# Performance work log

Hardware: AMD Instinct MI355X
Metric: run time of the kernel (lower is better)

## Reference

```python
import jax, jax.numpy as jnp
import numpy as np

NX = 96
N_NODES = 6 * NX * NX          # 55296 cubed-sphere grid points
N_EDGES = 4 * N_NODES          # ~4-neighbor connectivity
HID = 32
NUM_STEPS = 3


def setup_inputs() -> dict:
    key = jax.random.key(0)
    ks = jax.random.split(key, 12)
    s = 0.05
    inp = {
        "in_node_features": jax.random.normal(ks[0], (2, 6, NX, NX, 32), jnp.float32),
        "edge_relation": jax.random.normal(ks[1], (N_EDGES, 4), jnp.float32),
        "pw1": jax.random.normal(ks[2], (32, HID), jnp.float32) * s,
        "pb1": jnp.zeros((HID,), jnp.float32),
        "pw2": jax.random.normal(ks[3], (HID, HID), jnp.float32) * s,
        "pb2": jnp.zeros((HID,), jnp.float32),
        "ew1": jax.random.normal(ks[4], (4, 32), jnp.float32) * s,
        "eb1": jnp.zeros((32,), jnp.float32),
        "ew2": jax.random.normal(ks[5], (32, HID * HID), jnp.float32) * s,
        "eb2": jnp.zeros((HID * HID,), jnp.float32),
        "conv_b": jnp.zeros((HID,), jnp.float32),
        "gru_w_ih": jax.random.normal(ks[6], (3 * HID, HID), jnp.float32) * s,
        "gru_w_hh": jax.random.normal(ks[7], (3 * HID, HID), jnp.float32) * s,
        "gru_b_ih": jnp.zeros((3 * HID,), jnp.float32),
        "gru_b_hh": jnp.zeros((3 * HID,), jnp.float32),
        "edge_src": jax.random.randint(ks[8], (N_EDGES,), 0, N_NODES, jnp.int32),
        "edge_dst": jax.random.randint(ks[9], (N_EDGES,), 0, N_NODES, jnp.int32),
    }
    return inp


def reference(in_node_features, edge_relation, pw1, pb1, pw2, pb2,
              ew1, eb1, ew2, eb2, conv_b,
              gru_w_ih, gru_w_hh, gru_b_ih, gru_b_hh,
              edge_src, edge_dst):
    B, T, nx1, nx2, C = in_node_features.shape
    N = T * nx1 * nx2
    H = pw2.shape[1]

    x = in_node_features.reshape(B, N, C)
    # project_node_features: Linear -> ReLU -> Linear
    h0 = jnp.maximum(x @ pw1 + pb1, 0.0) @ pw2 + pb2          # [B, N, H]

    # edge network (same every step): Linear -> ReLU -> Linear -> [E, H, H]
    We = (jnp.maximum(edge_relation @ ew1 + eb1, 0.0) @ ew2 + eb2)
    We = We.reshape(-1, H, H)                                  # [E, H, H]

    def seg_sum(m):  # m: [E, H] -> [N, H]
        return jax.ops.segment_sum(m, edge_dst, num_segments=N)

    def step(carry, _):
        node, hidden = carry                                   # each [B, N, H]
        # NNConv: gather src feats, per-edge matmul, scatter-sum to dst
        msg = jnp.einsum('beh,eho->beo', node[:, edge_src], We)  # [B, E, H]
        agg = jax.vmap(seg_sum)(msg) + conv_b                    # [B, N, H]
        node = jnp.maximum(agg, 0.0)                             # ReLU
        # single GRU step (seq_len = 1)
        gx = node @ gru_w_ih.T + gru_b_ih                        # [B, N, 3H]
        gh = hidden @ gru_w_hh.T + gru_b_hh
        r = jax.nn.sigmoid(gx[..., :H] + gh[..., :H])
        z = jax.nn.sigmoid(gx[..., H:2 * H] + gh[..., H:2 * H])
        n = jnp.tanh(gx[..., 2 * H:] + r * gh[..., 2 * H:])
        hidden = (1.0 - z) * n + z * hidden
        return (hidden, hidden), None

    (node, _), _ = jax.lax.scan(step, (h0, h0), None, length=NUM_STEPS)
    return node.reshape(B, T, nx1, nx2, H)
```

## Files before the change

### kernel.cpp

```cpp
#include <hip/hip_runtime.h>

typedef unsigned short u16;
typedef short s16x8 __attribute__((ext_vector_type(8)));
typedef float f32x4 __attribute__((ext_vector_type(4)));
typedef float f32x2 __attribute__((ext_vector_type(2)));

#define NNODES 55296
#define NEDGES 221184
#define ROWS   110592
#define NBLK_SCAN 216

__device__ __forceinline__ u16 f2bf(float f) {
    union { float f; unsigned u; } v; v.f = f;
    unsigned r = (v.u + 0x7fffu + ((v.u >> 16) & 1u)) >> 16;
    return (u16)r;
}
__device__ __forceinline__ float bf2f(u16 u) {
    return __uint_as_float(((unsigned)u) << 16);
}

__global__ __launch_bounds__(256) void hist_kernel(
    const int* __restrict__ edst, int* __restrict__ cnt)
{
    int i = blockIdx.x * 256 + threadIdx.x;
    atomicAdd(&cnt[edst[i]], 1);
}

__global__ __launch_bounds__(256) void scan1_kernel(
    const int* __restrict__ cnt, int* __restrict__ exc, int* __restrict__ bsum)
{
    __shared__ int s[256];
    int t = threadIdx.x, g = blockIdx.x * 256 + t;
    int v = cnt[g];
    s[t] = v; __syncthreads();
#pragma unroll
    for (int d = 1; d < 256; d <<= 1) {
        int x = (t >= d) ? s[t - d] : 0;
        __syncthreads();
        s[t] += x;
        __syncthreads();
    }
    exc[g] = s[t] - v;
    if (t == 255) bsum[blockIdx.x] = s[255];
}

__global__ __launch_bounds__(256) void scan2_kernel(
    const int* __restrict__ bsum, int* __restrict__ bofs)
{
    __shared__ int s[256];
    int t = threadIdx.x;
    int v = (t < NBLK_SCAN) ? bsum[t] : 0;
    s[t] = v; __syncthreads();
#pragma unroll
    for (int d = 1; d < 256; d <<= 1) {
        int x = (t >= d) ? s[t - d] : 0;
        __syncthreads();
        s[t] += x;
        __syncthreads();
    }
    if (t < NBLK_SCAN) bofs[t] = s[t] - v;
}

__global__ __launch_bounds__(256) void scan3_kernel(
    const int* __restrict__ exc, const int* __restrict__ bofs, int* __restrict__ rowstart)
{
    int g = blockIdx.x * 256 + threadIdx.x;
    rowstart[g] = exc[g] + bofs[blockIdx.x];
    if (g == 0) rowstart[NNODES] = NEDGES;
}

__global__ __launch_bounds__(256) void scatter_kernel(
    const int* __restrict__ edst, const int* __restrict__ esrc,
    const int* __restrict__ rowstart, int* __restrict__ cursor,
    int* __restrict__ perm, int* __restrict__ esrcp, int* __restrict__ edstp)
{
    int i = blockIdx.x * 256 + threadIdx.x;
    int d = edst[i];
    int pos = rowstart[d] + atomicAdd(&cursor[d], 1);
    perm[pos] = i;
    esrcp[pos] = esrc[i];
    edstp[pos] = d;
}

__global__ __launch_bounds__(256) void pack_bfrag(
    const float* __restrict__ src, u16* __restrict__ dst_hi, u16* __restrict__ dst_lo,
    int ntiles, int ncols, int trans)
{
    int idx = blockIdx.x * 256 + threadIdx.x;
    if (idx >= ntiles * 512) return;
    int t = idx >> 9, rr = idx & 511, lane = rr >> 3, j = rr & 7;
    int k = (lane >> 4) * 8 + j;
    int n = t * 16 + (lane & 15);
    float v = trans ? src[n * 32 + k] : src[k * ncols + n];
    u16 hb = f2bf(v);
    dst_hi[idx] = hb;
    if (dst_lo) dst_lo[idx] = f2bf(v - bf2f(hb));
}

__global__ __launch_bounds__(256) void edgemlp_kernel(
    const float* __restrict__ er, const float* __restrict__ ew1,
    const float* __restrict__ eb1, const int* __restrict__ perm,
    u16* __restrict__ rbf)
{
    __shared__ float er_lds[32];
    __shared__ float w_lds[128];
    __shared__ float b_lds[32];
    int tid = threadIdx.x;
    int e8 = blockIdx.x * 8;
    if (tid < 32) {
        int e = perm[e8 + (tid >> 2)];
        er_lds[tid] = er[e * 4 + (tid & 3)];
    }
    else if (tid < 160) w_lds[tid - 32] = ew1[tid - 32];
    else if (tid < 192) b_lds[tid - 160] = eb1[tid - 160];
    __syncthreads();
    int el = tid >> 5, o = tid & 31;
    const float* e4 = er_lds + el * 4;
    float v = b_lds[o] + e4[0] * w_lds[o] + e4[1] * w_lds[32 + o]
                       + e4[2] * w_lds[64 + o] + e4[3] * w_lds[96 + o];
    rbf[(e8 + el) * 32 + o] = f2bf(fmaxf(v, 0.f));
}

__global__ __launch_bounds__(256) void nodeproj_kernel(
    const float* __restrict__ x,
    const u16* __restrict__ pw1h, const u16* __restrict__ pw1l, const float* __restrict__ pb1,
    const u16* __restrict__ pw2h, const u16* __restrict__ pw2l, const float* __restrict__ pb2,
    float* __restrict__ st_f32, u16* __restrict__ st_hi, u16* __restrict__ st_lo)
{
    __shared__ alignas(16) u16 t_hi[4][512];
    __shared__ alignas(16) u16 t_lo[4][512];
    int tid = threadIdx.x, wave = tid >> 6, lane = tid & 63;
    int quad = lane >> 4, col = lane & 15;
    int row0 = (blockIdx.x * 4 + wave) * 16;

    const float* xp = x + (row0 + col) * 32 + quad * 8;
    f32x4 xv0 = *(const f32x4*)(xp), xv1 = *(const f32x4*)(xp + 4);
    s16x8 ah, al;
#pragma unroll
    for (int i = 0; i < 4; ++i) {
        u16 h0 = f2bf(xv0[i]); ah[i] = (short)h0; al[i] = (short)f2bf(xv0[i] - bf2f(h0));
        u16 h1 = f2bf(xv1[i]); ah[4+i] = (short)h1; al[4+i] = (short)f2bf(xv1[i] - bf2f(h1));
    }
#pragma unroll
    for (int t = 0; t < 2; ++t) {
        s16x8 bh = *(const s16x8*)(pw1h + t * 512 + lane * 8);
        s16x8 bl = *(const s16x8*)(pw1l + t * 512 + lane * 8);
        f32x4 acc = {0,0,0,0};
        acc = __builtin_amdgcn_mfma_f32_16x16x32_bf16(al, bh, acc, 0,0,0);
        acc = __builtin_amdgcn_mfma_f32_16x16x32_bf16(ah, bl, acc, 0,0,0);
        acc = __builtin_amdgcn_mfma_f32_16x16x32_bf16(ah, bh, acc, 0,0,0);
        float bias = pb1[t * 16 + col];
#pragma unroll
        for (int r = 0; r < 4; ++r) {
            float v = fmaxf(acc[r] + bias, 0.f);
            u16 hb = f2bf(v);
            int idx = (quad * 4 + r) * 32 + t * 16 + col;
            t_hi[wave][idx] = hb;
            t_lo[wave][idx] = f2bf(v - bf2f(hb));
        }
    }
    __syncthreads();
    s16x8 th = *(const s16x8*)(&t_hi[wave][col * 32 + quad * 8]);
    s16x8 tl = *(const s16x8*)(&t_lo[wave][col * 32 + quad * 8]);
#pragma unroll
    for (int t = 0; t < 2; ++t) {
        s16x8 bh = *(const s16x8*)(pw2h + t * 512 + lane * 8);
        s16x8 bl = *(const s16x8*)(pw2l + t * 512 + lane * 8);
        f32x4 acc = {0,0,0,0};
        acc = __builtin_amdgcn_mfma_f32_16x16x32_bf16(tl, bh, acc, 0,0,0);
        acc = __builtin_amdgcn_mfma_f32_16x16x32_bf16(th, bl, acc, 0,0,0);
        acc = __builtin_amdgcn_mfma_f32_16x16x32_bf16(th, bh, acc, 0,0,0);
        float bias = pb2[t * 16 + col];
#pragma unroll
        for (int r = 0; r < 4; ++r) {
            float v = acc[r] + bias;
            int row = row0 + quad * 4 + r;
            int o = t * 16 + col;
            st_f32[row * 32 + o] = v;
            u16 hb = f2bf(v);
            st_hi[row * 32 + o] = hb;
            st_lo[row * 32 + o] = f2bf(v - bf2f(hb));
        }
    }
}

__global__ __launch_bounds__(256) void msg_kernel(
    const u16* __restrict__ rbf, const u16* __restrict__ ew2f,
    const float* __restrict__ eb2, const float* __restrict__ state,
    const int* __restrict__ esrcp, const int* __restrict__ edstp,
    float* __restrict__ agg)
{
    __shared__ alignas(16) float eb2_lds[1024];
    __shared__ alignas(16) float ns_lds[4][16 * 68];
    int tid = threadIdx.x;
    {
        *(f32x4*)(eb2_lds + tid * 4) = *(const f32x4*)(eb2 + tid * 4);
    }
    int wave = tid >> 6, lane = tid & 63;
    int quad = lane >> 4, col = lane & 15;
    int e0 = (blockIdx.x * 4 + wave) * 16;

    s16x8 afrag = *(const s16x8*)(rbf + (size_t)(e0 + col) * 32 + quad * 8);

    {
        int el = lane >> 2, part = lane & 3;
        int b = part >> 1, half = part & 1;
        int src = esrcp[e0 + el];
        const float* sp = state + (size_t)(b * NNODES + src) * 32 + half * 16;
        float* dp = &ns_lds[wave][el * 68 + b * 32 + half * 16];
        *(f32x4*)(dp + 0)  = *(const f32x4*)(sp + 0);
        *(f32x4*)(dp + 4)  = *(const f32x4*)(sp + 4);
        *(f32x4*)(dp + 8)  = *(const f32x4*)(sp + 8);
        *(f32x4*)(dp + 12) = *(const f32x4*)(sp + 12);
    }
    int dstid[4];
#pragma unroll
    for (int r = 0; r < 4; ++r) dstid[r] = edstp[e0 + quad * 4 + r];
    __syncthreads();

    float msg[2][2][4] = {};
    const float* nsw = &ns_lds[wave][0];
#pragma unroll 4
    for (int hh = 0; hh < 16; ++hh) {
        int h0 = hh * 2, h1 = hh * 2 + 1;
        s16x8 b0 = *(const s16x8*)(ew2f + (4 * hh + 0) * 512 + lane * 8);
        s16x8 b1 = *(const s16x8*)(ew2f + (4 * hh + 1) * 512 + lane * 8);
        s16x8 b2 = *(const s16x8*)(ew2f + (4 * hh + 2) * 512 + lane * 8);
        s16x8 b3 = *(const s16x8*)(ew2f + (4 * hh + 3) * 512 + lane * 8);
        f32x4 z = {0,0,0,0};
        f32x4 d0 = __builtin_amdgcn_mfma_f32_16x16x32_bf16(afrag, b0, z, 0,0,0);
        f32x4 d1 = __builtin_amdgcn_mfma_f32_16x16x32_bf16(afrag, b1, z, 0,0,0);
        f32x4 d2 = __builtin_amdgcn_mfma_f32_16x16x32_bf16(afrag, b2, z, 0,0,0);
        f32x4 d3 = __builtin_amdgcn_mfma_f32_16x16x32_bf16(afrag, b3, z, 0,0,0);
        float e00 = eb2_lds[h0 * 32 + col],      e01 = eb2_lds[h0 * 32 + 16 + col];
        float e10 = eb2_lds[h1 * 32 + col],      e11 = eb2_lds[h1 * 32 + 16 + col];
#pragma unroll
        for (int r = 0; r < 4; ++r) {
            int e = quad * 4 + r;
            f32x2 n0v = *(const f32x2*)(nsw + e * 68 + 0 * 32 + h0);
            f32x2 n1v = *(const f32x2*)(nsw + e * 68 + 1 * 32 + h0);
            float w00 = d0[r] + e00, w01 = d1[r] + e01;
            float w10 = d2[r] + e10, w11 = d3[r] + e11;
            msg[0][0][r] += n0v.x * w00 + n0v.y * w10;
            msg[0][1][r] += n0v.x * w01 + n0v.y * w11;
            msg[1][0][r] += n1v.x * w00 + n1v.y * w10;
            msg[1][1][r] += n1v.x * w01 + n1v.y * w11;
        }
    }
    bool valid[4] = {true, true, true, true};
#pragma unroll
    for (int r = 3; r >= 1; --r) {
        if (dstid[r] == dstid[r - 1]) {
            valid[r] = false;
            msg[0][0][r-1] += msg[0][0][r];
            msg[0][1][r-1] += msg[0][1][r];
            msg[1][0][r-1] += msg[1][0][r];
            msg[1][1][r-1] += msg[1][1][r];
        }
    }
#pragma unroll
    for (int r = 0; r < 4; ++r) {
        if (valid[r]) {
#pragma unroll
            for (int b = 0; b < 2; ++b) {
                float* base = agg + ((size_t)b * NNODES + dstid[r]) * 32;
                unsafeAtomicAdd(base + col,      msg[b][0][r]);
                unsafeAtomicAdd(base + 16 + col, msg[b][1][r]);
            }
        }
    }
}

__global__ __launch_bounds__(256) void gru_kernel(
    const float* __restrict__ agg, const float* __restrict__ conv_b,
    const float* __restrict__ st_f32, const u16* __restrict__ st_hi, const u16* __restrict__ st_lo,
    const u16* __restrict__ wihh, const u16* __restrict__ wihl,
    const u16* __restrict__ whhh, const u16* __restrict__ whhl,
    const float* __restrict__ b_ih, const float* __restrict__ b_hh,
    float* __restrict__ out_f32, u16* __restrict__ out_hi, u16* __restrict__ out_lo)
{
    int tid = threadIdx.x, wave = tid >> 6, lane = tid & 63;
    int quad = lane >> 4, col = lane & 15;
    int row0 = (blockIdx.x * 4 + wave) * 16;

    const float* ap = agg + (row0 + col) * 32 + quad * 8;
    f32x4 av0 = *(const f32x4*)(ap), av1 = *(const f32x4*)(ap + 4);
    const float* cb = conv_b + quad * 8;
    f32x4 cb0 = *(const f32x4*)(cb), cb1 = *(const f32x4*)(cb + 4);
    s16x8 anh, anl;
#pragma unroll
    for (int i = 0; i < 4; ++i) {
        float v0 = fmaxf(av0[i] + cb0[i], 0.f);
        float v1 = fmaxf(av1[i] + cb1[i], 0.f);
        u16 h0 = f2bf(v0); anh[i] = (short)h0;   anl[i] = (short)f2bf(v0 - bf2f(h0));
        u16 h1 = f2bf(v1); anh[4+i] = (short)h1; anl[4+i] = (short)f2bf(v1 - bf2f(h1));
    }
    s16x8 ahh = *(const s16x8*)(st_hi + (row0 + col) * 32 + quad * 8);
    s16x8 ahl = *(const s16x8*)(st_lo + (row0 + col) * 32 + quad * 8);

    f32x4 gx[6], gh[6];
#pragma unroll
    for (int t = 0; t < 6; ++t) {
        s16x8 bh = *(const s16x8*)(wihh + t * 512 + lane * 8);
        s16x8 bl = *(const s16x8*)(wihl + t * 512 + lane * 8);
        f32x4 acc = {0,0,0,0};
        acc = __builtin_amdgcn_mfma_f32_16x16x32_bf16(anl, bh, acc, 0,0,0);
        acc = __builtin_amdgcn_mfma_f32_16x16x32_bf16(anh, bl, acc, 0,0,0);
        acc = __builtin_amdgcn_mfma_f32_16x16x32_bf16(anh, bh, acc, 0,0,0);
        gx[t] = acc;
        s16x8 ch = *(const s16x8*)(whhh + t * 512 + lane * 8);
        s16x8 cl = *(const s16x8*)(whhl + t * 512 + lane * 8);
        f32x4 acc2 = {0,0,0,0};
        acc2 = __builtin_amdgcn_mfma_f32_16x16x32_bf16(ahl, ch, acc2, 0,0,0);
        acc2 = __builtin_amdgcn_mfma_f32_16x16x32_bf16(ahh, cl, acc2, 0,0,0);
        acc2 = __builtin_amdgcn_mfma_f32_16x16x32_bf16(ahh, ch, acc2, 0,0,0);
        gh[t] = acc2;
    }
    float bihv[6], bhhv[6];
#pragma unroll
    for (int t = 0; t < 6; ++t) { bihv[t] = b_ih[t * 16 + col]; bhhv[t] = b_hh[t * 16 + col]; }

#pragma unroll
    for (int r = 0; r < 4; ++r) {
        int row = row0 + quad * 4 + r;
#pragma unroll
        for (int oh = 0; oh < 2; ++oh) {
            int o = oh * 16 + col;
            float hid = st_f32[row * 32 + o];
            float sr = (gx[oh][r] + bihv[oh]) + (gh[oh][r] + bhhv[oh]);
            float sz = (gx[2+oh][r] + bihv[2+oh]) + (gh[2+oh][r] + bhhv[2+oh]);
            float gxn = gx[4+oh][r] + bihv[4+oh];
            float ghn = gh[4+oh][r] + bhhv[4+oh];
            float rr = 1.f / (1.f + __expf(-sr));
            float zz = 1.f / (1.f + __expf(-sz));
            float narg = gxn + rr * ghn;
            float ex = __expf(2.f * narg);
            float nn = (ex - 1.f) / (ex + 1.f);
            float hnew = (1.f - zz) * nn + zz * hid;
            out_f32[row * 32 + o] = hnew;
            u16 hb = f2bf(hnew);
            out_hi[row * 32 + o] = hb;
            out_lo[row * 32 + o] = f2bf(hnew - bf2f(hb));
        }
    }
}

extern "C" void kernel_launch(void* const* d_in, const int* in_sizes, int n_in,
                              void* d_out, int out_size, void* d_ws, size_t ws_size,
                              hipStream_t stream)
{
    const float* x      = (const float*)d_in[0];
    const float* er     = (const float*)d_in[1];
    const float* pw1    = (const float*)d_in[2];
    const float* pb1    = (const float*)d_in[3];
    const float* pw2    = (const float*)d_in[4];
    const float* pb2    = (const float*)d_in[5];
    const float* ew1    = (const float*)d_in[6];
    const float* eb1    = (const float*)d_in[7];
    const float* ew2    = (const float*)d_in[8];
    const float* eb2    = (const float*)d_in[9];
    const float* conv_b = (const float*)d_in[10];
    const float* wih    = (const float*)d_in[11];
    const float* whh    = (const float*)d_in[12];
    const float* bih    = (const float*)d_in[13];
    const float* bhh    = (const float*)d_in[14];
    const int*   esrc   = (const int*)d_in[15];
    const int*   edst   = (const int*)d_in[16];
    float* out = (float*)d_out;

    char* ws = (char*)d_ws;
    size_t off = 0;
    auto alloc = [&](size_t bytes) -> void* {
        void* p = ws + off;
        off = (off + bytes + 255) & ~(size_t)255;
        return p;
    };
    u16*   rbf    = (u16*)  alloc((size_t)(NEDGES + 16) * 32 * 2);
    float* st_f32 = (float*)alloc((size_t)ROWS * 32 * 4);
    u16*   st_hi  = (u16*)  alloc((size_t)ROWS * 32 * 2);
    u16*   st_lo  = (u16*)  alloc((size_t)ROWS * 32 * 2);
    float* agg    = (float*)alloc((size_t)ROWS * 32 * 4);
    u16*   ew2f   = (u16*)  alloc(64 * 512 * 2);
    u16*   pw1h   = (u16*)  alloc(2 * 512 * 2);
    u16*   pw1l   = (u16*)  alloc(2 * 512 * 2);
    u16*   pw2h   = (u16*)  alloc(2 * 512 * 2);
    u16*   pw2l   = (u16*)  alloc(2 * 512 * 2);
    u16*   wihhf  = (u16*)  alloc(6 * 512 * 2);
    u16*   wihlf  = (u16*)  alloc(6 * 512 * 2);
    u16*   whhhf  = (u16*)  alloc(6 * 512 * 2);
    u16*   whhlf  = (u16*)  alloc(6 * 512 * 2);
    int*   cnt      = (int*)alloc((size_t)NNODES * 4);
    int*   cursor   = (int*)alloc((size_t)NNODES * 4);
    int*   exc      = (int*)alloc((size_t)NNODES * 4);
    int*   bsum     = (int*)alloc(NBLK_SCAN * 4);
    int*   bofs     = (int*)alloc(NBLK_SCAN * 4);
    int*   rowstart = (int*)alloc((size_t)(NNODES + 1) * 4);
    int*   perm     = (int*)alloc((size_t)NEDGES * 4);
    int*   esrcp    = (int*)alloc((size_t)(NEDGES + 16) * 4);
    int*   edstp    = (int*)alloc((size_t)(NEDGES + 16) * 4);
    (void)in_sizes; (void)n_in; (void)out_size; (void)ws_size;

    hipMemsetAsync(cnt, 0, (size_t)NNODES * 4, stream);
    hipMemsetAsync(cursor, 0, (size_t)NNODES * 4, stream);
    hist_kernel<<<NEDGES / 256, 256, 0, stream>>>(edst, cnt);
    scan1_kernel<<<NBLK_SCAN, 256, 0, stream>>>(cnt, exc, bsum);
    scan2_kernel<<<1, 256, 0, stream>>>(bsum, bofs);
    scan3_kernel<<<NBLK_SCAN, 256, 0, stream>>>(exc, bofs, rowstart);
    scatter_kernel<<<NEDGES / 256, 256, 0, stream>>>(edst, esrc, rowstart, cursor,
                                                     perm, esrcp, edstp);

    pack_bfrag<<<128, 256, 0, stream>>>(ew2, ew2f, (u16*)nullptr, 64, 1024, 0);
    pack_bfrag<<<4,   256, 0, stream>>>(pw1, pw1h, pw1l, 2, 32, 0);
    pack_bfrag<<<4,   256, 0, stream>>>(pw2, pw2h, pw2l, 2, 32, 0);
    pack_bfrag<<<12,  256, 0, stream>>>(wih, wihhf, wihlf, 6, 96, 1);
    pack_bfrag<<<12,  256, 0, stream>>>(whh, whhhf, whhlf, 6, 96, 1);

    edgemlp_kernel<<<NEDGES / 8, 256, 0, stream>>>(er, ew1, eb1, perm, rbf);
    nodeproj_kernel<<<ROWS / 64, 256, 0, stream>>>(x, pw1h, pw1l, pb1, pw2h, pw2l, pb2,
                                                   st_f32, st_hi, st_lo);
    for (int s = 0; s < 3; ++s) {
        hipMemsetAsync(agg, 0, (size_t)ROWS * 32 * 4, stream);
        msg_kernel<<<NEDGES / 64, 256, 0, stream>>>(rbf, ew2f, eb2, st_f32,
                                                    esrcp, edstp, agg);
        float* of = (s == 2) ? out : st_f32;
        gru_kernel<<<ROWS / 64, 256, 0, stream>>>(agg, conv_b, st_f32, st_hi, st_lo,
                                                  wihhf, wihlf, whhhf, whhlf, bih, bhh,
                                                  of, st_hi, st_lo);
    }
}
```

Measured before the change: 386.7 us.

## Process 32 edges per wave in msg kernel and fuse setup kernels

The message kernel now handles 32 edges per wave instead of 16. Each ew2 B-fragment load is reused across two MFMA tiles, and the two batch copies of each source node are interleaved in LDS so one 128-bit read serves both batches with packed f32x2 math. The CSR build drops the scan3 kernel, the cursor memset and the rowstart array by decrementing the histogram counts atomically and computing offsets inline. The five weight-packing launches become one kernel. The cost is more registers and LDS per wave, which may lower occupancy, and the order of edges within each destination segment changes.

```diff
diff --git a/kernel.cpp b/kernel.cpp
--- a/kernel.cpp
+++ b/kernel.cpp
@@ -61,40 +61,43 @@
     if (t < NBLK_SCAN) bofs[t] = s[t] - v;
 }
 
-__global__ __launch_bounds__(256) void scan3_kernel(
-    const int* __restrict__ exc, const int* __restrict__ bofs, int* __restrict__ rowstart)
-{
-    int g = blockIdx.x * 256 + threadIdx.x;
-    rowstart[g] = exc[g] + bofs[blockIdx.x];
-    if (g == 0) rowstart[NNODES] = NEDGES;
-}
-
 __global__ __launch_bounds__(256) void scatter_kernel(
     const int* __restrict__ edst, const int* __restrict__ esrc,
-    const int* __restrict__ rowstart, int* __restrict__ cursor,
+    const int* __restrict__ exc, const int* __restrict__ bofs,
+    int* __restrict__ cnt,
     int* __restrict__ perm, int* __restrict__ esrcp, int* __restrict__ edstp)
 {
     int i = blockIdx.x * 256 + threadIdx.x;
     int d = edst[i];
-    int pos = rowstart[d] + atomicAdd(&cursor[d], 1);
+    int slot = atomicSub(&cnt[d], 1) - 1;
+    int pos = exc[d] + bofs[d >> 8] + slot;
     perm[pos] = i;
     esrcp[pos] = esrc[i];
     edstp[pos] = d;
 }
 
-__global__ __launch_bounds__(256) void pack_bfrag(
-    const float* __restrict__ src, u16* __restrict__ dst_hi, u16* __restrict__ dst_lo,
-    int ntiles, int ncols, int trans)
-{
-    int idx = blockIdx.x * 256 + threadIdx.x;
-    if (idx >= ntiles * 512) return;
+__global__ __launch_bounds__(256) void pack_all(
+    const float* __restrict__ ew2, u16* __restrict__ ew2f,
+    const float* __restrict__ pw1, u16* __restrict__ pw1h, u16* __restrict__ pw1l,
+    const float* __restrict__ pw2, u16* __restrict__ pw2h, u16* __restrict__ pw2l,
+    const float* __restrict__ wih, u16* __restrict__ wihh, u16* __restrict__ wihl,
+    const float* __restrict__ whh, u16* __restrict__ whhh, u16* __restrict__ whhl)
+{
+    int b = blockIdx.x;
+    const float* src; u16 *hi, *lo; int ncols, trans, base;
+    if (b < 128)      { src = ew2; hi = ew2f; lo = nullptr; ncols = 1024; trans = 0; base = 0;   }
+    else if (b < 132) { src = pw1; hi = pw1h; lo = pw1l;    ncols = 32;   trans = 0; base = 128; }
+    else if (b < 136) { src = pw2; hi = pw2h; lo = pw2l;    ncols = 32;   trans = 0; base = 132; }
+    else if (b < 148) { src = wih; hi = wihh; lo = wihl;    ncols = 96;   trans = 1; base = 136; }
+    else              { src = whh; hi = whhh; lo = whhl;    ncols = 96;   trans = 1; base = 148; }
+    int idx = (b - base) * 256 + threadIdx.x;
     int t = idx >> 9, rr = idx & 511, lane = rr >> 3, j = rr & 7;
     int k = (lane >> 4) * 8 + j;
     int n = t * 16 + (lane & 15);
     float v = trans ? src[n * 32 + k] : src[k * ncols + n];
     u16 hb = f2bf(v);
-    dst_hi[idx] = hb;
-    if (dst_lo) dst_lo[idx] = f2bf(v - bf2f(hb));
+    hi[idx] = hb;
+    if (lo) lo[idx] = f2bf(v - bf2f(hb));
 }
 
 __global__ __launch_bounds__(256) void edgemlp_kernel(
@@ -191,36 +194,55 @@
     float* __restrict__ agg)
 {
     __shared__ alignas(16) float eb2_lds[1024];
-    __shared__ alignas(16) float ns_lds[4][16 * 68];
+    __shared__ alignas(16) float ns_lds[4][32 * 68];
     int tid = threadIdx.x;
     {
         *(f32x4*)(eb2_lds + tid * 4) = *(const f32x4*)(eb2 + tid * 4);
     }
     int wave = tid >> 6, lane = tid & 63;
     int quad = lane >> 4, col = lane & 15;
-    int e0 = (blockIdx.x * 4 + wave) * 16;
-
-    s16x8 afrag = *(const s16x8*)(rbf + (size_t)(e0 + col) * 32 + quad * 8);
-
-    {
-        int el = lane >> 2, part = lane & 3;
-        int b = part >> 1, half = part & 1;
+    int e0 = (blockIdx.x * 4 + wave) * 32;
+
+    s16x8 afrag0 = *(const s16x8*)(rbf + (size_t)(e0 + col) * 32 + quad * 8);
+    s16x8 afrag1 = *(const s16x8*)(rbf + (size_t)(e0 + 16 + col) * 32 + quad * 8);
+
+#pragma unroll
+    for (int i = 0; i < 2; ++i) {
+        int t2 = i * 64 + lane;
+        int el = t2 >> 2, hc = t2 & 3;
         int src = esrcp[e0 + el];
-        const float* sp = state + (size_t)(b * NNODES + src) * 32 + half * 16;
-        float* dp = &ns_lds[wave][el * 68 + b * 32 + half * 16];
-        *(f32x4*)(dp + 0)  = *(const f32x4*)(sp + 0);
-        *(f32x4*)(dp + 4)  = *(const f32x4*)(sp + 4);
-        *(f32x4*)(dp + 8)  = *(const f32x4*)(sp + 8);
-        *(f32x4*)(dp + 12) = *(const f32x4*)(sp + 12);
-    }
-    int dstid[4];
-#pragma unroll
-    for (int r = 0; r < 4; ++r) dstid[r] = edstp[e0 + quad * 4 + r];
+        const float* s0 = state + (size_t)src * 32 + hc * 8;
+        const float* s1 = state + ((size_t)NNODES + src) * 32 + hc * 8;
+        f32x4 a0 = *(const f32x4*)(s0),     a1 = *(const f32x4*)(s0 + 4);
+        f32x4 c0 = *(const f32x4*)(s1),     c1 = *(const f32x4*)(s1 + 4);
+        float* dp = &ns_lds[wave][el * 68 + hc * 16];
+        f32x4 w0 = {a0.x, c0.x, a0.y, c0.y};
+        f32x4 w1 = {a0.z, c0.z, a0.w, c0.w};
+        f32x4 w2 = {a1.x, c1.x, a1.y, c1.y};
+        f32x4 w3 = {a1.z, c1.z, a1.w, c1.w};
+        *(f32x4*)(dp + 0)  = w0;
+        *(f32x4*)(dp + 4)  = w1;
+        *(f32x4*)(dp + 8)  = w2;
+        *(f32x4*)(dp + 12) = w3;
+    }
+    int dstid[8];
+#pragma unroll
+    for (int g = 0; g < 2; ++g)
+#pragma unroll
+        for (int r = 0; r < 4; ++r)
+            dstid[g * 4 + r] = edstp[e0 + g * 16 + quad * 4 + r];
     __syncthreads();
 
-    float msg[2][2][4] = {};
+    f32x2 m[2][2][4];
+#pragma unroll
+    for (int g = 0; g < 2; ++g)
+#pragma unroll
+        for (int oh = 0; oh < 2; ++oh)
+#pragma unroll
+            for (int r = 0; r < 4; ++r) m[g][oh][r] = f32x2{0.f, 0.f};
+
     const float* nsw = &ns_lds[wave][0];
-#pragma unroll 4
+#pragma unroll 2
     for (int hh = 0; hh < 16; ++hh) {
         int h0 = hh * 2, h1 = hh * 2 + 1;
         s16x8 b0 = *(const s16x8*)(ew2f + (4 * hh + 0) * 512 + lane * 8);
@@ -228,44 +250,52 @@
         s16x8 b2 = *(const s16x8*)(ew2f + (4 * hh + 2) * 512 + lane * 8);
         s16x8 b3 = *(const s16x8*)(ew2f + (4 * hh + 3) * 512 + lane * 8);
         f32x4 z = {0,0,0,0};
-        f32x4 d0 = __builtin_amdgcn_mfma_f32_16x16x32_bf16(afrag, b0, z, 0,0,0);
-        f32x4 d1 = __builtin_amdgcn_mfma_f32_16x16x32_bf16(afrag, b1, z, 0,0,0);
-        f32x4 d2 = __builtin_amdgcn_mfma_f32_16x16x32_bf16(afrag, b2, z, 0,0,0);
-        f32x4 d3 = __builtin_amdgcn_mfma_f32_16x16x32_bf16(afrag, b3, z, 0,0,0);
-        float e00 = eb2_lds[h0 * 32 + col],      e01 = eb2_lds[h0 * 32 + 16 + col];
-        float e10 = eb2_lds[h1 * 32 + col],      e11 = eb2_lds[h1 * 32 + 16 + col];
+        f32x4 d[2][4];
+        d[0][0] = __builtin_amdgcn_mfma_f32_16x16x32_bf16(afrag0, b0, z, 0,0,0);
+        d[0][1] = __builtin_amdgcn_mfma_f32_16x16x32_bf16(afrag0, b1, z, 0,0,0);
+        d[0][2] = __builtin_amdgcn_mfma_f32_16x16x32_bf16(afrag0, b2, z, 0,0,0);
+        d[0][3] = __builtin_amdgcn_mfma_f32_16x16x32_bf16(afrag0, b3, z, 0,0,0);
+        d[1][0] = __builtin_amdgcn_mfma_f32_16x16x32_bf16(afrag1, b0, z, 0,0,0);
+        d[1][1] = __builtin_amdgcn_mfma_f32_16x16x32_bf16(afrag1, b1, z, 0,0,0);
+        d[1][2] = __builtin_amdgcn_mfma_f32_16x16x32_bf16(afrag1, b2, z, 0,0,0);
+        d[1][3] = __builtin_amdgcn_mfma_f32_16x16x32_bf16(afrag1, b3, z, 0,0,0);
+        float e00 = eb2_lds[h0 * 32 + col],  e01 = eb2_lds[h0 * 32 + 16 + col];
+        float e10 = eb2_lds[h1 * 32 + col],  e11 = eb2_lds[h1 * 32 + 16 + col];
+#pragma unroll
+        for (int g = 0; g < 2; ++g) {
+#pragma unroll
+            for (int r = 0; r < 4; ++r) {
+                int e = g * 16 + quad * 4 + r;
+                f32x4 nv = *(const f32x4*)(nsw + e * 68 + hh * 4);
+                f32x2 nh0 = {nv.x, nv.y};
+                f32x2 nh1 = {nv.z, nv.w};
+                float w00 = d[g][0][r] + e00, w01 = d[g][1][r] + e01;
+                float w10 = d[g][2][r] + e10, w11 = d[g][3][r] + e11;
+                m[g][0][r] += nh0 * w00 + nh1 * w10;
+                m[g][1][r] += nh0 * w01 + nh1 * w11;
+            }
+        }
+    }
+#pragma unroll
+    for (int g = 0; g < 2; ++g) {
+        bool valid[4] = {true, true, true, true};
+#pragma unroll
+        for (int r = 3; r >= 1; --r) {
+            if (dstid[g * 4 + r] == dstid[g * 4 + r - 1]) {
+                valid[r] = false;
+                m[g][0][r-1] += m[g][0][r];
+                m[g][1][r-1] += m[g][1][r];
+            }
+        }
 #pragma unroll
         for (int r = 0; r < 4; ++r) {
-            int e = quad * 4 + r;
-            f32x2 n0v = *(const f32x2*)(nsw + e * 68 + 0 * 32 + h0);
-            f32x2 n1v = *(const f32x2*)(nsw + e * 68 + 1 * 32 + h0);
-            float w00 = d0[r] + e00, w01 = d1[r] + e01;
-            float w10 = d2[r] + e10, w11 = d3[r] + e11;
-            msg[0][0][r] += n0v.x * w00 + n0v.y * w10;
-            msg[0][1][r] += n0v.x * w01 + n0v.y * w11;
-            msg[1][0][r] += n1v.x * w00 + n1v.y * w10;
-            msg[1][1][r] += n1v.x * w01 + n1v.y * w11;
-        }
-    }
-    bool valid[4] = {true, true, true, true};
-#pragma unroll
-    for (int r = 3; r >= 1; --r) {
-        if (dstid[r] == dstid[r - 1]) {
-            valid[r] = false;
-            msg[0][0][r-1] += msg[0][0][r];
-            msg[0][1][r-1] += msg[0][1][r];
-            msg[1][0][r-1] += msg[1][0][r];
-            msg[1][1][r-1] += msg[1][1][r];
-        }
-    }
-#pragma unroll
-    for (int r = 0; r < 4; ++r) {
-        if (valid[r]) {
-#pragma unroll
-            for (int b = 0; b < 2; ++b) {
-                float* base = agg + ((size_t)b * NNODES + dstid[r]) * 32;
-                unsafeAtomicAdd(base + col,      msg[b][0][r]);
-                unsafeAtomicAdd(base + 16 + col, msg[b][1][r]);
+            if (valid[r]) {
+                float* p0 = agg + (size_t)dstid[g * 4 + r] * 32;
+                float* p1 = agg + ((size_t)NNODES + dstid[g * 4 + r]) * 32;
+                unsafeAtomicAdd(p0 + col,      m[g][0][r].x);
+                unsafeAtomicAdd(p0 + 16 + col, m[g][1][r].x);
+                unsafeAtomicAdd(p1 + col,      m[g][0][r].y);
+                unsafeAtomicAdd(p1 + 16 + col, m[g][1][r].y);
             }
         }
     }
@@ -375,7 +405,7 @@
         off = (off + bytes + 255) & ~(size_t)255;
         return p;
     };
-    u16*   rbf    = (u16*)  alloc((size_t)(NEDGES + 16) * 32 * 2);
+    u16*   rbf    = (u16*)  alloc((size_t)(NEDGES + 32) * 32 * 2);
     float* st_f32 = (float*)alloc((size_t)ROWS * 32 * 4);
     u16*   st_hi  = (u16*)  alloc((size_t)ROWS * 32 * 2);
     u16*   st_lo  = (u16*)  alloc((size_t)ROWS * 32 * 2);
@@ -390,38 +420,31 @@
     u16*   whhhf  = (u16*)  alloc(6 * 512 * 2);
     u16*   whhlf  = (u16*)  alloc(6 * 512 * 2);
     int*   cnt      = (int*)alloc((size_t)NNODES * 4);
-    int*   cursor   = (int*)alloc((size_t)NNODES * 4);
     int*   exc      = (int*)alloc((size_t)NNODES * 4);
     int*   bsum     = (int*)alloc(NBLK_SCAN * 4);
     int*   bofs     = (int*)alloc(NBLK_SCAN * 4);
-    int*   rowstart = (int*)alloc((size_t)(NNODES + 1) * 4);
     int*   perm     = (int*)alloc((size_t)NEDGES * 4);
-    int*   esrcp    = (int*)alloc((size_t)(NEDGES + 16) * 4);
-    int*   edstp    = (int*)alloc((size_t)(NEDGES + 16) * 4);
+    int*   esrcp    = (int*)alloc((size_t)(NEDGES + 32) * 4);
+    int*   edstp    = (int*)alloc((size_t)(NEDGES + 32) * 4);
     (void)in_sizes; (void)n_in; (void)out_size; (void)ws_size;
 
     hipMemsetAsync(cnt, 0, (size_t)NNODES * 4, stream);
-    hipMemsetAsync(cursor, 0, (size_t)NNODES * 4, stream);
     hist_kernel<<<NEDGES / 256, 256, 0, stream>>>(edst, cnt);
     scan1_kernel<<<NBLK_SCAN, 256, 0, stream>>>(cnt, exc, bsum);
     scan2_kernel<<<1, 256, 0, stream>>>(bsum, bofs);
-    scan3_kernel<<<NBLK_SCAN, 256, 0, stream>>>(exc, bofs, rowstart);
-    scatter_kernel<<<NEDGES / 256, 256, 0, stream>>>(edst, esrc, rowstart, cursor,
+    scatter_kernel<<<NEDGES / 256, 256, 0, stream>>>(edst, esrc, exc, bofs, cnt,
                                                      perm, esrcp, edstp);
 
-    pack_bfrag<<<128, 256, 0, stream>>>(ew2, ew2f, (u16*)nullptr, 64, 1024, 0);
-    pack_bfrag<<<4,   256, 0, stream>>>(pw1, pw1h, pw1l, 2, 32, 0);
-    pack_bfrag<<<4,   256, 0, stream>>>(pw2, pw2h, pw2l, 2, 32, 0);
-    pack_bfrag<<<12,  256, 0, stream>>>(wih, wihhf, wihlf, 6, 96, 1);
-    pack_bfrag<<<12,  256, 0, stream>>>(whh, whhhf, whhlf, 6, 96, 1);
+    pack_all<<<160, 256, 0, stream>>>(ew2, ew2f, pw1, pw1h, pw1l, pw2, pw2h, pw2l,
+                                      wih, wihhf, wihlf, whh, whhhf, whhlf);
 
     edgemlp_kernel<<<NEDGES / 8, 256, 0, stream>>>(er, ew1, eb1, perm, rbf);
     nodeproj_kernel<<<ROWS / 64, 256, 0, stream>>>(x, pw1h, pw1l, pb1, pw2h, pw2l, pb2,
                                                    st_f32, st_hi, st_lo);
     for (int s = 0; s < 3; ++s) {
         hipMemsetAsync(agg, 0, (size_t)ROWS * 32 * 4, stream);
-        msg_kernel<<<NEDGES / 64, 256, 0, stream>>>(rbf, ew2f, eb2, st_f32,
-                                                    esrcp, edstp, agg);
+        msg_kernel<<<NEDGES / 128, 256, 0, stream>>>(rbf, ew2f, eb2, st_f32,
+                                                     esrcp, edstp, agg);
         float* of = (s == 2) ? out : st_f32;
         gru_kernel<<<ROWS / 64, 256, 0, stream>>>(agg, conv_b, st_f32, st_hi, st_lo,
                                                   wihhf, wihlf, whhhf, whhlf, bih, bhh,
```

Measured after the change: 379.4 us. No clear change (-1.9%).
